# Kernel optimization log

Measured on AMD Instinct MI355X. Metric: run time of the kernel, lower is better.

## Reference

```python
import jax, jax.numpy as jnp
import numpy as np

RES = 512
RANK = 48
OUT = 32
N = 1_000_000
INIT = 0.1


def _contract_linf(xyz, aabb):
    # L-infinity cuboid contraction of unbounded coords into [-1,1]^3.
    center = (aabb[:3] + aabb[3:]) * 0.5
    half = jnp.maximum((aabb[3:] - aabb[:3]) * 0.5, 1e-6)
    x = (xyz - center) / half
    linf = jnp.max(jnp.abs(x), axis=-1, keepdims=True)
    safe = jnp.maximum(linf, 1.0)
    scale = jnp.where(linf > 1.0, (2.0 - 1.0 / safe) / safe, 1.0)
    return jnp.clip(x * scale, -1.0, 1.0)


def _sample_plane(plane, gx, gy):
    # plane: [R, Res, Res]; gx,gy in [-1,1] shape [N]; bilinear, align_corners=True.
    res = plane.shape[-1]
    fx = (gx + 1.0) * 0.5 * (res - 1)
    fy = (gy + 1.0) * 0.5 * (res - 1)
    x0 = jnp.clip(jnp.floor(fx), 0, res - 2).astype(jnp.int32)
    y0 = jnp.clip(jnp.floor(fy), 0, res - 2).astype(jnp.int32)
    wx = fx - x0
    wy = fy - y0
    x1 = x0 + 1
    y1 = y0 + 1
    # gathers -> [R, N]
    v = (plane[:, y0, x0] * ((1 - wy) * (1 - wx))
         + plane[:, y0, x1] * ((1 - wy) * wx)
         + plane[:, y1, x0] * (wy * (1 - wx))
         + plane[:, y1, x1] * (wy * wx))
    return v


def _sample_line(line, g):
    # line: [R, Res]; 1-D linear interp along the resolution axis (align_corners=True).
    res = line.shape[-1]
    f = (g + 1.0) * 0.5 * (res - 1)
    i0 = jnp.clip(jnp.floor(f), 0, res - 2).astype(jnp.int32)
    w = f - i0
    return line[:, i0] * (1 - w) + line[:, i0 + 1] * w  # [R, N]


def setup_inputs() -> dict:
    key = jax.random.key(0)
    ks = jax.random.split(key, 9)
    coordinates = jax.random.normal(ks[0], (N, 3), dtype=jnp.float32) * 1.5  # some points outside aabb
    aabb = jnp.array([-1.0, -1.0, -1.0, 1.0, 1.0, 1.0], dtype=jnp.float32)
    plane_xy = jax.random.normal(ks[1], (RANK, RES, RES), dtype=jnp.float32) * INIT
    plane_xz = jax.random.normal(ks[2], (RANK, RES, RES), dtype=jnp.float32) * INIT
    plane_yz = jax.random.normal(ks[3], (RANK, RES, RES), dtype=jnp.float32) * INIT
    line_z = jax.random.normal(ks[4], (RANK, RES), dtype=jnp.float32) * INIT
    line_y = jax.random.normal(ks[5], (RANK, RES), dtype=jnp.float32) * INIT
    line_x = jax.random.normal(ks[6], (RANK, RES), dtype=jnp.float32) * INIT
    W = jax.random.normal(ks[7], (OUT, RANK), dtype=jnp.float32) * INIT
    b = jnp.zeros((OUT,), dtype=jnp.float32)
    return {"coordinates": coordinates, "aabb": aabb,
            "plane_xy": plane_xy, "plane_xz": plane_xz, "plane_yz": plane_yz,
            "line_z": line_z, "line_y": line_y, "line_x": line_x,
            "W": W, "b": b}


def reference(coordinates, aabb, plane_xy, plane_xz, plane_yz, line_z, line_y, line_x, W, b):
    c = _contract_linf(coordinates, aabb)  # [N,3] in [-1,1]
    cx, cy, cz = c[:, 0], c[:, 1], c[:, 2]
    # VM decomposition: plane(a,b) * line(c), summed over the three permutations -> [R, N]
    vm = (_sample_plane(plane_xy, cx, cy) * _sample_line(line_z, cz)
          + _sample_plane(plane_xz, cx, cz) * _sample_line(line_y, cy)
          + _sample_plane(plane_yz, cy, cz) * _sample_line(line_x, cx))
    # projection rank -> out_channels: [N, OUT]
    return jnp.einsum('rn,or->no', vm, W) + b
```

## Files before the change

### kernel.cpp

```cpp
#include <hip/hip_runtime.h>
#include <stdint.h>

#define RES 512
#define RANK 48
#define OUT_CH 32
#define KBITS 5
#define NBKT (1 << (3 * KBITS))
#define STR 24

typedef unsigned int u32;
typedef unsigned short u16;
typedef u32 u32x4 __attribute__((ext_vector_type(4)));


static __device__ __forceinline__ u16 f2bf(float f){
  u32 u = __float_as_uint(f);
  u32 r = (u + 0x7fffu + ((u >> 16) & 1u)) >> 16;
  return (u16)r;
}

struct PS { int off; float w00, w01, w10, w11; };
static __device__ __forceinline__ PS plane_setup(float gx, float gy){
  float fx = (gx + 1.f) * 255.5f;
  float fy = (gy + 1.f) * 255.5f;
  float x0f = fminf(fmaxf(floorf(fx), 0.f), 510.f);
  float y0f = fminf(fmaxf(floorf(fy), 0.f), 510.f);
  float wx = fx - x0f, wy = fy - y0f;
  PS s;
  s.off = (int)y0f * RES + (int)x0f;
  float ux = 1.f - wx, uy = 1.f - wy;
  s.w00 = uy * ux; s.w01 = uy * wx; s.w10 = wy * ux; s.w11 = wy * wx;
  return s;
}

struct LS { int off; float w; };
static __device__ __forceinline__ LS line_setup(float g){
  float f = (g + 1.f) * 255.5f;
  float i0f = fminf(fmaxf(floorf(f), 0.f), 510.f);
  LS s; s.off = (int)i0f; s.w = f - i0f;
  return s;
}

static __device__ __forceinline__ void contract(const float* __restrict__ aabb,
                                                float px, float py, float pz,
                                                float& cx, float& cy, float& cz){
  float c0 = (aabb[0] + aabb[3]) * 0.5f;
  float c1 = (aabb[1] + aabb[4]) * 0.5f;
  float c2 = (aabb[2] + aabb[5]) * 0.5f;
  float h0 = fmaxf((aabb[3] - aabb[0]) * 0.5f, 1e-6f);
  float h1 = fmaxf((aabb[4] - aabb[1]) * 0.5f, 1e-6f);
  float h2 = fmaxf((aabb[5] - aabb[2]) * 0.5f, 1e-6f);
  float x0 = (px - c0) / h0;
  float x1 = (py - c1) / h1;
  float x2 = (pz - c2) / h2;
  float linf = fmaxf(fabsf(x0), fmaxf(fabsf(x1), fabsf(x2)));
  float scale = 1.f;
  if (linf > 1.f){ float inv = 1.f / linf; scale = (2.f - inv) * inv; }
  cx = fminf(fmaxf(x0 * scale, -1.f), 1.f);
  cy = fminf(fmaxf(x1 * scale, -1.f), 1.f);
  cz = fminf(fmaxf(x2 * scale, -1.f), 1.f);
}

static __device__ __forceinline__ u32 spread3(u32 x){
  x &= 0x3FF;
  x = (x | (x << 16)) & 0x030000FF;
  x = (x | (x <<  8)) & 0x0300F00F;
  x = (x | (x <<  4)) & 0x030C30C3;
  x = (x | (x <<  2)) & 0x09249249;
  return x;
}

static __device__ __forceinline__ u32 morton_key(float cx, float cy, float cz){
  u32 kx = (u32)fminf(fmaxf((cx + 1.f) * 16.f, 0.f), 31.f);
  u32 ky = (u32)fminf(fmaxf((cy + 1.f) * 16.f, 0.f), 31.f);
  u32 kz = (u32)fminf(fmaxf((cz + 1.f) * 16.f, 0.f), 31.f);
  return spread3(kx) | (spread3(ky) << 1) | (spread3(kz) << 2);
}


__global__ void zero_hist(u32* __restrict__ hist)
{
  hist[blockIdx.x * 1024 + threadIdx.x] = 0u;
}


#define TRANS_P 3072
#define TRANS_L 6

__global__ void prep_fused(const float* __restrict__ pxy, const float* __restrict__ pxz,
                           const float* __restrict__ pyz,
                           const float* __restrict__ lz, const float* __restrict__ ly,
                           const float* __restrict__ lx,
                           const float* __restrict__ coords, const float* __restrict__ aabb,
                           u32* __restrict__ dstP, u32* __restrict__ dstL,
                           u32* __restrict__ hist, u32* __restrict__ keyrank, int n)
{
  __shared__ u32 lds[256 * 25];
  int bid = blockIdx.x;
  int tid = threadIdx.x;
  if (bid < TRANS_P){
    int xh = bid & 1, y = (bid >> 1) & 511, p = bid >> 10;
    const float* src = (p == 0) ? pxy : (p == 1) ? pxz : pyz;
    int x = xh * 256 + tid;
    #pragma unroll
    for (int r2 = 0; r2 < 24; ++r2){
      float f0 = src[((size_t)(2 * r2) * RES + y) * RES + x];
      float f1 = src[((size_t)(2 * r2 + 1) * RES + y) * RES + x];
      lds[tid * 25 + r2] = (u32)f2bf(f0) | ((u32)f2bf(f1) << 16);
    }
    __syncthreads();
    u32* dplane = dstP + (size_t)p * (RES * RES * STR);
    size_t base = ((size_t)y * RES + xh * 256) * STR;
    for (int t = tid; t < 256 * STR; t += 256){
      dplane[base + t] = lds[t + t / 24];
    }
  } else if (bid < TRANS_P + TRANS_L){
    int g = (bid - TRANS_P) * 256 + tid;
    if (g < 3 * RES){
      int p = g >> 9, i = g & 511;
      const float* src = (p == 0) ? lz : (p == 1) ? ly : lx;
      u32* d = dstL + (size_t)g * STR;
      #pragma unroll
      for (int r2 = 0; r2 < 24; ++r2){
        float f0 = src[(2 * r2) * RES + i];
        float f1 = src[(2 * r2 + 1) * RES + i];
        d[r2] = (u32)f2bf(f0) | ((u32)f2bf(f1) << 16);
      }
    }
  } else {
    int i = (bid - TRANS_P - TRANS_L) * 256 + tid;
    if (i < n){
      float cx, cy, cz;
      contract(aabb, coords[3*i], coords[3*i+1], coords[3*i+2], cx, cy, cz);
      u32 key = morton_key(cx, cy, cz);
      u32 rank = atomicAdd(hist + key, 1u);
      keyrank[i] = (rank << 15) | key;
    }
  }
}


__global__ void scan_kernel(u32* __restrict__ hist)
{
  __shared__ u32 part[1024];
  int tid = threadIdx.x;
  int base = tid * 32;
  u32 loc[32];
  u32 s = 0;
  #pragma unroll
  for (int j = 0; j < 32; j++){ loc[j] = hist[base + j]; s += loc[j]; }
  part[tid] = s;
  __syncthreads();
  for (int off = 1; off < 1024; off <<= 1){
    u32 v = 0;
    if (tid >= off) v = part[tid - off];
    __syncthreads();
    part[tid] += v;
    __syncthreads();
  }
  u32 run = part[tid] - s;
  #pragma unroll
  for (int j = 0; j < 32; j++){ u32 t = loc[j]; hist[base + j] = run; run += t; }
}


__global__ void key_scatter(const float* __restrict__ coords, const float* __restrict__ aabb,
                            const u32* __restrict__ base, const u32* __restrict__ keyrank,
                            float4* __restrict__ sorted, int n)
{
  int i = blockIdx.x * 256 + threadIdx.x;
  if (i >= n) return;
  float cx, cy, cz;
  contract(aabb, coords[3*i], coords[3*i+1], coords[3*i+2], cx, cy, cz);
  u32 kr = keyrank[i];
  u32 pos = base[kr & 0x7FFFu] + (kr >> 15);
  sorted[pos] = make_float4(cx, cy, cz, __uint_as_float((u32)i));
}


#define EXLO(u) __uint_as_float((u) << 16)
#define EXHI(u) __uint_as_float((u) & 0xffff0000u)

#define DO_ELEM(EX, RIDX) do{ \
  float pa = fmaf(EX(a00[jj]), sa.w00, fmaf(EX(a01[jj]), sa.w01, fmaf(EX(a10[jj]), sa.w10, EX(a11[jj]) * sa.w11))); \
  float pb = fmaf(EX(b00[jj]), sb.w00, fmaf(EX(b01[jj]), sb.w01, fmaf(EX(b10[jj]), sb.w10, EX(b11[jj]) * sb.w11))); \
  float pc = fmaf(EX(c00[jj]), sc.w00, fmaf(EX(c01[jj]), sc.w01, fmaf(EX(c10[jj]), sc.w10, EX(c11[jj]) * sc.w11))); \
  float lzv = fmaf(tz.w, EX(vz1[jj]) - EX(vz0[jj]), EX(vz0[jj])); \
  float lyv = fmaf(ty.w, EX(vy1[jj]) - EX(vy0[jj]), EX(vy0[jj])); \
  float lxv = fmaf(tx.w, EX(vx1[jj]) - EX(vx0[jj]), EX(vx0[jj])); \
  float vm = fmaf(pa, lzv, fmaf(pb, lyv, pc * lxv)); \
  const float4* wrow = Wt4 + (RIDX) * 8; \
  _Pragma("unroll") for (int q = 0; q < 8; q++){ float4 w4 = wrow[q]; \
    acc[4*q+0] = fmaf(vm, w4.x, acc[4*q+0]); acc[4*q+1] = fmaf(vm, w4.y, acc[4*q+1]); \
    acc[4*q+2] = fmaf(vm, w4.z, acc[4*q+2]); acc[4*q+3] = fmaf(vm, w4.w, acc[4*q+3]); } \
}while(0)

static __device__ __forceinline__ void geo_compute(float cx, float cy, float cz,
    const u32* __restrict__ pl, const u32* __restrict__ ln,
    const float* __restrict__ Wt, const float* __restrict__ bias,
    float* __restrict__ acc)
{
  PS sa = plane_setup(cx, cy);
  PS sb = plane_setup(cx, cz);
  PS sc = plane_setup(cy, cz);
  LS tz = line_setup(cz);
  LS ty = line_setup(cy);
  LS tx = line_setup(cx);

  const u32* P0 = pl + (size_t)sa.off * STR;
  const u32* P1 = pl + (size_t)RES * RES * STR     + (size_t)sb.off * STR;
  const u32* P2 = pl + (size_t)2 * RES * RES * STR + (size_t)sc.off * STR;
  const u32* LZp = ln +                          (size_t)tz.off * STR;
  const u32* LYp = ln + (size_t)RES * STR     + (size_t)ty.off * STR;
  const u32* LXp = ln + (size_t)2 * RES * STR + (size_t)tx.off * STR;

  #pragma unroll
  for (int o = 0; o < 8; o++){
    float4 bv = *(const float4*)(bias + o * 4);
    acc[4*o+0] = bv.x; acc[4*o+1] = bv.y; acc[4*o+2] = bv.z; acc[4*o+3] = bv.w;
  }
  const float4* Wt4 = (const float4*)Wt;

  #pragma unroll 2
  for (int ch = 0; ch < 6; ++ch){
    const int bo = ch * 4;
    u32x4 a00 = *(const u32x4*)(P0 + bo);
    u32x4 a01 = *(const u32x4*)(P0 + STR + bo);
    u32x4 a10 = *(const u32x4*)(P0 + RES * STR + bo);
    u32x4 a11 = *(const u32x4*)(P0 + RES * STR + STR + bo);
    u32x4 b00 = *(const u32x4*)(P1 + bo);
    u32x4 b01 = *(const u32x4*)(P1 + STR + bo);
    u32x4 b10 = *(const u32x4*)(P1 + RES * STR + bo);
    u32x4 b11 = *(const u32x4*)(P1 + RES * STR + STR + bo);
    u32x4 c00 = *(const u32x4*)(P2 + bo);
    u32x4 c01 = *(const u32x4*)(P2 + STR + bo);
    u32x4 c10 = *(const u32x4*)(P2 + RES * STR + bo);
    u32x4 c11 = *(const u32x4*)(P2 + RES * STR + STR + bo);
    u32x4 vz0 = *(const u32x4*)(LZp + bo);
    u32x4 vz1 = *(const u32x4*)(LZp + STR + bo);
    u32x4 vy0 = *(const u32x4*)(LYp + bo);
    u32x4 vy1 = *(const u32x4*)(LYp + STR + bo);
    u32x4 vx0 = *(const u32x4*)(LXp + bo);
    u32x4 vx1 = *(const u32x4*)(LXp + STR + bo);

    #pragma unroll
    for (int jj = 0; jj < 4; jj++){
      DO_ELEM(EXLO, ch * 8 + jj * 2);
      DO_ELEM(EXHI, ch * 8 + jj * 2 + 1);
    }
  }
}


__global__ __launch_bounds__(256, 2)
void geo_sorted(const float4* __restrict__ sorted,
                const u32* __restrict__ pl, const u32* __restrict__ ln,
                const float* __restrict__ W, const float* __restrict__ bias,
                float* __restrict__ out, int n, int nwg)
{
  __shared__ __align__(16) float Wt[RANK * OUT_CH];
  for (int t = threadIdx.x; t < RANK * OUT_CH; t += 256){
    int r = t >> 5, o = t & 31;
    Wt[t] = W[o * RANK + r];
  }
  __syncthreads();

  int bid = blockIdx.x;
  int q = nwg >> 3, r8 = nwg & 7;
  int xcd = bid & 7, sub = bid >> 3;
  int swz = (xcd < r8 ? xcd * (q + 1) : r8 * (q + 1) + (xcd - r8) * q) + sub;

  int i = swz * 256 + threadIdx.x;
  if (i >= n) return;

  u32x4 pr = __builtin_nontemporal_load((const u32x4*)(sorted + i));
  float cx = __uint_as_float(pr[0]);
  float cy = __uint_as_float(pr[1]);
  float cz = __uint_as_float(pr[2]);
  u32 oidx = pr[3];

  float acc[OUT_CH];
  geo_compute(cx, cy, cz, pl, ln, Wt, bias, acc);

  float4* o4 = (float4*)(out + (size_t)oidx * 32);
  #pragma unroll
  for (int qq = 0; qq < 8; qq++)
    o4[qq] = make_float4(acc[4*qq+0], acc[4*qq+1], acc[4*qq+2], acc[4*qq+3]);
}


__global__ __launch_bounds__(256, 2)
void geo_unsorted(const float* __restrict__ coords, const float* __restrict__ aabb,
                  const u32* __restrict__ pl, const u32* __restrict__ ln,
                  const float* __restrict__ W, const float* __restrict__ bias,
                  float* __restrict__ out, int n)
{
  __shared__ __align__(16) float Wt[RANK * OUT_CH];
  for (int t = threadIdx.x; t < RANK * OUT_CH; t += 256){
    int r = t >> 5, o = t & 31;
    Wt[t] = W[o * RANK + r];
  }
  __syncthreads();

  int i = blockIdx.x * 256 + threadIdx.x;
  if (i >= n) return;

  float cx, cy, cz;
  contract(aabb, coords[3*i], coords[3*i+1], coords[3*i+2], cx, cy, cz);

  float acc[OUT_CH];
  geo_compute(cx, cy, cz, pl, ln, Wt, bias, acc);

  float4* o4 = (float4*)(out + (size_t)i * 32);
  #pragma unroll
  for (int qq = 0; qq < 8; qq++)
    o4[qq] = make_float4(acc[4*qq+0], acc[4*qq+1], acc[4*qq+2], acc[4*qq+3]);
}


__global__ __launch_bounds__(256, 2)
void geo_direct(const float* __restrict__ coords, const float* __restrict__ aabb,
                const float* __restrict__ PXY, const float* __restrict__ PXZ, const float* __restrict__ PYZ,
                const float* __restrict__ LZ, const float* __restrict__ LY, const float* __restrict__ LX,
                const float* __restrict__ W, const float* __restrict__ bias,
                float* __restrict__ out, int n)
{
  __shared__ __align__(16) float Wt[RANK * OUT_CH];
  for (int t = threadIdx.x; t < RANK * OUT_CH; t += 256){
    int r = t >> 5, o = t & 31;
    Wt[t] = W[o * RANK + r];
  }
  __syncthreads();

  int i = blockIdx.x * 256 + threadIdx.x;
  if (i >= n) return;

  float cx, cy, cz;
  contract(aabb, coords[3*i], coords[3*i+1], coords[3*i+2], cx, cy, cz);

  PS sa = plane_setup(cx, cy);
  PS sb = plane_setup(cx, cz);
  PS sc = plane_setup(cy, cz);
  LS tz = line_setup(cz);
  LS ty = line_setup(cy);
  LS tx = line_setup(cx);

  float acc[OUT_CH];
  #pragma unroll
  for (int o = 0; o < 8; o++){
    float4 bv = *(const float4*)(bias + o * 4);
    acc[4*o+0] = bv.x; acc[4*o+1] = bv.y; acc[4*o+2] = bv.z; acc[4*o+3] = bv.w;
  }
  const float4* Wt4 = (const float4*)Wt;

  for (int r = 0; r < RANK; r++){
    const float* pA = PXY + (size_t)r * RES * RES;
    const float* pB = PXZ + (size_t)r * RES * RES;
    const float* pC = PYZ + (size_t)r * RES * RES;
    float va = fmaf(pA[sa.off], sa.w00, fmaf(pA[sa.off+1], sa.w01, fmaf(pA[sa.off+RES], sa.w10, pA[sa.off+RES+1]*sa.w11)));
    float vb = fmaf(pB[sb.off], sb.w00, fmaf(pB[sb.off+1], sb.w01, fmaf(pB[sb.off+RES], sb.w10, pB[sb.off+RES+1]*sb.w11)));
    float vc = fmaf(pC[sc.off], sc.w00, fmaf(pC[sc.off+1], sc.w01, fmaf(pC[sc.off+RES], sc.w10, pC[sc.off+RES+1]*sc.w11)));
    float l0;
    l0 = LZ[r * RES + tz.off];
    float lzv = fmaf(tz.w, LZ[r * RES + tz.off + 1] - l0, l0);
    l0 = LY[r * RES + ty.off];
    float lyv = fmaf(ty.w, LY[r * RES + ty.off + 1] - l0, l0);
    l0 = LX[r * RES + tx.off];
    float lxv = fmaf(tx.w, LX[r * RES + tx.off + 1] - l0, l0);
    float vm = fmaf(va, lzv, fmaf(vb, lyv, vc * lxv));
    const float4* wrow = Wt4 + r * 8;
    #pragma unroll
    for (int q = 0; q < 8; q++){
      float4 w4 = wrow[q];
      acc[4*q+0] = fmaf(vm, w4.x, acc[4*q+0]); acc[4*q+1] = fmaf(vm, w4.y, acc[4*q+1]);
      acc[4*q+2] = fmaf(vm, w4.z, acc[4*q+2]); acc[4*q+3] = fmaf(vm, w4.w, acc[4*q+3]);
    }
  }

  float4* o4 = (float4*)(out + (size_t)i * 32);
  #pragma unroll
  for (int q = 0; q < 8; q++)
    o4[q] = make_float4(acc[4*q+0], acc[4*q+1], acc[4*q+2], acc[4*q+3]);
}


extern "C" void kernel_launch(void* const* d_in, const int* in_sizes, int n_in,
                              void* d_out, int out_size, void* d_ws, size_t ws_size,
                              hipStream_t stream)
{
  const float* coords = (const float*)d_in[0];
  const float* aabb   = (const float*)d_in[1];
  const float* pxy    = (const float*)d_in[2];
  const float* pxz    = (const float*)d_in[3];
  const float* pyz    = (const float*)d_in[4];
  const float* lz     = (const float*)d_in[5];
  const float* ly     = (const float*)d_in[6];
  const float* lx     = (const float*)d_in[7];
  const float* W      = (const float*)d_in[8];
  const float* bias   = (const float*)d_in[9];
  float* out = (float*)d_out;
  int n = in_sizes[0] / 3;
  int nwg = (n + 255) / 256;

  const size_t planesU = (size_t)3 * RES * RES * STR;
  const size_t linesU  = (size_t)3 * RES * STR;
  const size_t histU   = NBKT;
  const size_t keyrU   = (size_t)n;
  const size_t sortedU = (size_t)4 * n;
  const size_t needFull = (planesU + linesU + histU + keyrU + sortedU) * 4;

  if (ws_size >= needFull){
    u32* pl      = (u32*)d_ws;
    u32* ln      = pl + planesU;
    u32* hist    = ln + linesU;
    u32* keyrank = hist + histU;
    float4* sorted = (float4*)(keyrank + keyrU);
    zero_hist<<<NBKT / 1024, 1024, 0, stream>>>(hist);
    prep_fused<<<TRANS_P + TRANS_L + nwg, 256, 0, stream>>>(
        pxy, pxz, pyz, lz, ly, lx, coords, aabb, pl, ln, hist, keyrank, n);
    scan_kernel<<<1, 1024, 0, stream>>>(hist);
    key_scatter<<<nwg, 256, 0, stream>>>(coords, aabb, hist, keyrank, sorted, n);
    geo_sorted<<<nwg, 256, 0, stream>>>(sorted, pl, ln, W, bias, out, n, nwg);
  } else if (ws_size >= (planesU + linesU) * 4){
    u32* pl = (u32*)d_ws;
    u32* ln = pl + planesU;
    prep_fused<<<TRANS_P + TRANS_L, 256, 0, stream>>>(
        pxy, pxz, pyz, lz, ly, lx, coords, aabb, pl, ln, (u32*)pl, (u32*)pl, 0);
    geo_unsorted<<<nwg, 256, 0, stream>>>(coords, aabb, pl, ln, W, bias, out, n);
  } else {
    geo_direct<<<nwg, 256, 0, stream>>>(coords, aabb, pxy, pxz, pyz, lz, ly, lx, W, bias, out, n);
  }
}
```

Before: 413.8 us.

## Bucket points by clamped-axis class and skip zero-weight corner loads

Points are classified by whether a contracted coordinate sits exactly on a clamped boundary, where one bilinear or linear weight is exactly 0 or 1. That class goes into the sort key ahead of the Morton code, so wavefronts are grouped by class. The kernel then picks a templated specialization per wavefront that skips the gather loads for zero-weight plane corners and line endpoints. This cuts memory gathers for the many points outside the box, whose contraction lands on the boundary. In exchange the histogram is seven times larger, the scan is wider, and key and rank now go to separate arrays, all of which add prep traffic.

New measurement: 869.6 us. 110% more time.

```diff
diff --git a/kernel.cpp b/kernel.cpp
--- a/kernel.cpp
+++ b/kernel.cpp
@@ -5,7 +5,9 @@
 #define RANK 48
 #define OUT_CH 32
 #define KBITS 5
-#define NBKT (1 << (3 * KBITS))
+#define NMORT (1 << (3 * KBITS))
+#define NCLS 7
+#define NBKT2 (NCLS * NMORT)
 #define STR 24
 
 typedef unsigned int u32;
@@ -19,26 +21,10 @@
   return (u16)r;
 }
 
-struct PS { int off; float w00, w01, w10, w11; };
-static __device__ __forceinline__ PS plane_setup(float gx, float gy){
-  float fx = (gx + 1.f) * 255.5f;
-  float fy = (gy + 1.f) * 255.5f;
-  float x0f = fminf(fmaxf(floorf(fx), 0.f), 510.f);
-  float y0f = fminf(fmaxf(floorf(fy), 0.f), 510.f);
-  float wx = fx - x0f, wy = fy - y0f;
-  PS s;
-  s.off = (int)y0f * RES + (int)x0f;
-  float ux = 1.f - wx, uy = 1.f - wy;
-  s.w00 = uy * ux; s.w01 = uy * wx; s.w10 = wy * ux; s.w11 = wy * wx;
-  return s;
-}
-
-struct LS { int off; float w; };
-static __device__ __forceinline__ LS line_setup(float g){
-  float f = (g + 1.f) * 255.5f;
-  float i0f = fminf(fmaxf(floorf(f), 0.f), 510.f);
-  LS s; s.off = (int)i0f; s.w = f - i0f;
-  return s;
+static __device__ __forceinline__ void axis_setup(float c, int& o, float& w){
+  float f = (c + 1.f) * 255.5f;
+  float of = fminf(fmaxf(floorf(f), 0.f), 510.f);
+  o = (int)of; w = f - of;
 }
 
 static __device__ __forceinline__ void contract(const float* __restrict__ aabb,
@@ -77,6 +63,12 @@
   return spread3(kx) | (spread3(ky) << 1) | (spread3(kz) << 2);
 }
 
+static __device__ __forceinline__ u32 classify(float wx, float wy, float wz){
+  return (wx == 1.f) ? 0u : (wx == 0.f) ? 1u :
+         (wy == 1.f) ? 2u : (wy == 0.f) ? 3u :
+         (wz == 1.f) ? 4u : (wz == 0.f) ? 5u : 6u;
+}
+
 
 __global__ void zero_hist(u32* __restrict__ hist)
 {
@@ -93,7 +85,8 @@
                            const float* __restrict__ lx,
                            const float* __restrict__ coords, const float* __restrict__ aabb,
                            u32* __restrict__ dstP, u32* __restrict__ dstL,
-                           u32* __restrict__ hist, u32* __restrict__ keyrank, int n)
+                           u32* __restrict__ hist, u32* __restrict__ keyA,
+                           u32* __restrict__ rankA, int n)
 {
   __shared__ u32 lds[256 * 25];
   int bid = blockIdx.x;
@@ -132,9 +125,11 @@
     if (i < n){
       float cx, cy, cz;
       contract(aabb, coords[3*i], coords[3*i+1], coords[3*i+2], cx, cy, cz);
-      u32 key = morton_key(cx, cy, cz);
-      u32 rank = atomicAdd(hist + key, 1u);
-      keyrank[i] = (rank << 15) | key;
+      int ox, oy, oz; float wx, wy, wz;
+      axis_setup(cx, ox, wx); axis_setup(cy, oy, wy); axis_setup(cz, oz, wz);
+      u32 key = (classify(wx, wy, wz) << 15) | morton_key(cx, cy, cz);
+      keyA[i] = key;
+      rankA[i] = atomicAdd(hist + key, 1u);
     }
   }
 }
@@ -143,12 +138,11 @@
 __global__ void scan_kernel(u32* __restrict__ hist)
 {
   __shared__ u32 part[1024];
+  const int PER4 = NBKT2 / 1024 / 4;
   int tid = threadIdx.x;
-  int base = tid * 32;
-  u32 loc[32];
+  uint4* h4 = (uint4*)hist + (size_t)tid * PER4;
   u32 s = 0;
-  #pragma unroll
-  for (int j = 0; j < 32; j++){ loc[j] = hist[base + j]; s += loc[j]; }
+  for (int j = 0; j < PER4; ++j){ uint4 v = h4[j]; s += v.x + v.y + v.z + v.w; }
   part[tid] = s;
   __syncthreads();
   for (int off = 1; off < 1024; off <<= 1){
@@ -159,21 +153,26 @@
     __syncthreads();
   }
   u32 run = part[tid] - s;
-  #pragma unroll
-  for (int j = 0; j < 32; j++){ u32 t = loc[j]; hist[base + j] = run; run += t; }
+  for (int j = 0; j < PER4; ++j){
+    uint4 v = h4[j], o;
+    o.x = run; run += v.x;
+    o.y = run; run += v.y;
+    o.z = run; run += v.z;
+    o.w = run; run += v.w;
+    h4[j] = o;
+  }
 }
 
 
 __global__ void key_scatter(const float* __restrict__ coords, const float* __restrict__ aabb,
-                            const u32* __restrict__ base, const u32* __restrict__ keyrank,
-                            float4* __restrict__ sorted, int n)
+                            const u32* __restrict__ base, const u32* __restrict__ keyA,
+                            const u32* __restrict__ rankA, float4* __restrict__ sorted, int n)
 {
   int i = blockIdx.x * 256 + threadIdx.x;
   if (i >= n) return;
   float cx, cy, cz;
   contract(aabb, coords[3*i], coords[3*i+1], coords[3*i+2], cx, cy, cz);
-  u32 kr = keyrank[i];
-  u32 pos = base[kr & 0x7FFFu] + (kr >> 15);
+  u32 pos = base[keyA[i]] + rankA[i];
   sorted[pos] = make_float4(cx, cy, cz, __uint_as_float((u32)i));
 }
 
@@ -181,13 +180,16 @@
 #define EXLO(u) __uint_as_float((u) << 16)
 #define EXHI(u) __uint_as_float((u) & 0xffff0000u)
 
+#define LOADC(name, FLAG, addr) \
+  u32x4 name = {0,0,0,0}; if constexpr (FLAG){ name = *(const u32x4*)(addr); }
+
 #define DO_ELEM(EX, RIDX) do{ \
-  float pa = fmaf(EX(a00[jj]), sa.w00, fmaf(EX(a01[jj]), sa.w01, fmaf(EX(a10[jj]), sa.w10, EX(a11[jj]) * sa.w11))); \
-  float pb = fmaf(EX(b00[jj]), sb.w00, fmaf(EX(b01[jj]), sb.w01, fmaf(EX(b10[jj]), sb.w10, EX(b11[jj]) * sb.w11))); \
-  float pc = fmaf(EX(c00[jj]), sc.w00, fmaf(EX(c01[jj]), sc.w01, fmaf(EX(c10[jj]), sc.w10, EX(c11[jj]) * sc.w11))); \
-  float lzv = fmaf(tz.w, EX(vz1[jj]) - EX(vz0[jj]), EX(vz0[jj])); \
-  float lyv = fmaf(ty.w, EX(vy1[jj]) - EX(vy0[jj]), EX(vy0[jj])); \
-  float lxv = fmaf(tx.w, EX(vx1[jj]) - EX(vx0[jj]), EX(vx0[jj])); \
+  float pa = fmaf(EX(a00[jj]), aw00, fmaf(EX(a01[jj]), aw01, fmaf(EX(a10[jj]), aw10, EX(a11[jj]) * aw11))); \
+  float pb = fmaf(EX(b00[jj]), bw00, fmaf(EX(b01[jj]), bw01, fmaf(EX(b10[jj]), bw10, EX(b11[jj]) * bw11))); \
+  float pc = fmaf(EX(c00[jj]), cw00, fmaf(EX(c01[jj]), cw01, fmaf(EX(c10[jj]), cw10, EX(c11[jj]) * cw11))); \
+  float lzv = fmaf(wz, EX(vz1[jj]) - EX(vz0[jj]), EX(vz0[jj])); \
+  float lyv = fmaf(wy, EX(vy1[jj]) - EX(vy0[jj]), EX(vy0[jj])); \
+  float lxv = fmaf(wx, EX(vx1[jj]) - EX(vx0[jj]), EX(vx0[jj])); \
   float vm = fmaf(pa, lzv, fmaf(pb, lyv, pc * lxv)); \
   const float4* wrow = Wt4 + (RIDX) * 8; \
   _Pragma("unroll") for (int q = 0; q < 8; q++){ float4 w4 = wrow[q]; \
@@ -195,24 +197,37 @@
     acc[4*q+2] = fmaf(vm, w4.z, acc[4*q+2]); acc[4*q+3] = fmaf(vm, w4.w, acc[4*q+3]); } \
 }while(0)
 
-static __device__ __forceinline__ void geo_compute(float cx, float cy, float cz,
+template<int CLS>
+static __device__ __forceinline__ void geo_core(int ox, int oy, int oz,
+    float wx, float wy, float wz,
     const u32* __restrict__ pl, const u32* __restrict__ ln,
     const float* __restrict__ Wt, const float* __restrict__ bias,
     float* __restrict__ acc)
 {
-  PS sa = plane_setup(cx, cy);
-  PS sb = plane_setup(cx, cz);
-  PS sc = plane_setup(cy, cz);
-  LS tz = line_setup(cz);
-  LS ty = line_setup(cy);
-  LS tx = line_setup(cx);
-
-  const u32* P0 = pl + (size_t)sa.off * STR;
-  const u32* P1 = pl + (size_t)RES * RES * STR     + (size_t)sb.off * STR;
-  const u32* P2 = pl + (size_t)2 * RES * RES * STR + (size_t)sc.off * STR;
-  const u32* LZp = ln +                          (size_t)tz.off * STR;
-  const u32* LYp = ln + (size_t)RES * STR     + (size_t)ty.off * STR;
-  const u32* LXp = ln + (size_t)2 * RES * STR + (size_t)tx.off * STR;
+  constexpr bool SXP = (CLS == 0), SXM = (CLS == 1);
+  constexpr bool SYP = (CLS == 2), SYM = (CLS == 3);
+  constexpr bool SZP = (CLS == 4), SZM = (CLS == 5);
+  constexpr bool LA00 = !(SXP || SYP), LA01 = !(SXM || SYP);
+  constexpr bool LA10 = !(SXP || SYM), LA11 = !(SXM || SYM);
+  constexpr bool LB00 = !(SXP || SZP), LB01 = !(SXM || SZP);
+  constexpr bool LB10 = !(SXP || SZM), LB11 = !(SXM || SZM);
+  constexpr bool LC00 = !(SYP || SZP), LC01 = !(SYM || SZP);
+  constexpr bool LC10 = !(SYP || SZM), LC11 = !(SYM || SZM);
+  constexpr bool LZ0 = !SZP, LZ1 = !SZM;
+  constexpr bool LY0 = !SYP, LY1 = !SYM;
+  constexpr bool LX0 = !SXP, LX1 = !SXM;
+
+  float uxw = 1.f - wx, uyw = 1.f - wy, uzw = 1.f - wz;
+  float aw00 = uyw * uxw, aw01 = uyw * wx, aw10 = wy * uxw, aw11 = wy * wx;
+  float bw00 = uzw * uxw, bw01 = uzw * wx, bw10 = wz * uxw, bw11 = wz * wx;
+  float cw00 = uzw * uyw, cw01 = uzw * wy, cw10 = wz * uyw, cw11 = wz * wy;
+
+  const u32* P0 = pl + ((size_t)oy * RES + ox) * STR;
+  const u32* P1 = pl + (size_t)RES * RES * STR     + ((size_t)oz * RES + ox) * STR;
+  const u32* P2 = pl + (size_t)2 * RES * RES * STR + ((size_t)oz * RES + oy) * STR;
+  const u32* LZp = ln +                          (size_t)oz * STR;
+  const u32* LYp = ln + (size_t)RES * STR     + (size_t)oy * STR;
+  const u32* LXp = ln + (size_t)2 * RES * STR + (size_t)ox * STR;
 
   #pragma unroll
   for (int o = 0; o < 8; o++){
@@ -224,24 +239,24 @@
   #pragma unroll 2
   for (int ch = 0; ch < 6; ++ch){
     const int bo = ch * 4;
-    u32x4 a00 = *(const u32x4*)(P0 + bo);
-    u32x4 a01 = *(const u32x4*)(P0 + STR + bo);
-    u32x4 a10 = *(const u32x4*)(P0 + RES * STR + bo);
-    u32x4 a11 = *(const u32x4*)(P0 + RES * STR + STR + bo);
-    u32x4 b00 = *(const u32x4*)(P1 + bo);
-    u32x4 b01 = *(const u32x4*)(P1 + STR + bo);
-    u32x4 b10 = *(const u32x4*)(P1 + RES * STR + bo);
-    u32x4 b11 = *(const u32x4*)(P1 + RES * STR + STR + bo);
-    u32x4 c00 = *(const u32x4*)(P2 + bo);
-    u32x4 c01 = *(const u32x4*)(P2 + STR + bo);
-    u32x4 c10 = *(const u32x4*)(P2 + RES * STR + bo);
-    u32x4 c11 = *(const u32x4*)(P2 + RES * STR + STR + bo);
-    u32x4 vz0 = *(const u32x4*)(LZp + bo);
-    u32x4 vz1 = *(const u32x4*)(LZp + STR + bo);
-    u32x4 vy0 = *(const u32x4*)(LYp + bo);
-    u32x4 vy1 = *(const u32x4*)(LYp + STR + bo);
-    u32x4 vx0 = *(const u32x4*)(LXp + bo);
-    u32x4 vx1 = *(const u32x4*)(LXp + STR + bo);
+    LOADC(a00, LA00, P0 + bo);
+    LOADC(a01, LA01, P0 + STR + bo);
+    LOADC(a10, LA10, P0 + RES * STR + bo);
+    LOADC(a11, LA11, P0 + RES * STR + STR + bo);
+    LOADC(b00, LB00, P1 + bo);
+    LOADC(b01, LB01, P1 + STR + bo);
+    LOADC(b10, LB10, P1 + RES * STR + bo);
+    LOADC(b11, LB11, P1 + RES * STR + STR + bo);
+    LOADC(c00, LC00, P2 + bo);
+    LOADC(c01, LC01, P2 + STR + bo);
+    LOADC(c10, LC10, P2 + RES * STR + bo);
+    LOADC(c11, LC11, P2 + RES * STR + STR + bo);
+    LOADC(vz0, LZ0, LZp + bo);
+    LOADC(vz1, LZ1, LZp + STR + bo);
+    LOADC(vy0, LY0, LYp + bo);
+    LOADC(vy1, LY1, LYp + STR + bo);
+    LOADC(vx0, LX0, LXp + bo);
+    LOADC(vx1, LX1, LXp + STR + bo);
 
     #pragma unroll
     for (int jj = 0; jj < 4; jj++){
@@ -279,8 +294,17 @@
   float cz = __uint_as_float(pr[2]);
   u32 oidx = pr[3];
 
+  int ox, oy, oz; float wx, wy, wz;
+  axis_setup(cx, ox, wx); axis_setup(cy, oy, wy); axis_setup(cz, oz, wz);
+
   float acc[OUT_CH];
-  geo_compute(cx, cy, cz, pl, ln, Wt, bias, acc);
+  if      (__all(wx == 1.f)) geo_core<0>(ox, oy, oz, wx, wy, wz, pl, ln, Wt, bias, acc);
+  else if (__all(wx == 0.f)) geo_core<1>(ox, oy, oz, wx, wy, wz, pl, ln, Wt, bias, acc);
+  else if (__all(wy == 1.f)) geo_core<2>(ox, oy, oz, wx, wy, wz, pl, ln, Wt, bias, acc);
+  else if (__all(wy == 0.f)) geo_core<3>(ox, oy, oz, wx, wy, wz, pl, ln, Wt, bias, acc);
+  else if (__all(wz == 1.f)) geo_core<4>(ox, oy, oz, wx, wy, wz, pl, ln, Wt, bias, acc);
+  else if (__all(wz == 0.f)) geo_core<5>(ox, oy, oz, wx, wy, wz, pl, ln, Wt, bias, acc);
+  else                       geo_core<6>(ox, oy, oz, wx, wy, wz, pl, ln, Wt, bias, acc);
 
   float4* o4 = (float4*)(out + (size_t)oidx * 32);
   #pragma unroll
@@ -307,9 +331,11 @@
 
   float cx, cy, cz;
   contract(aabb, coords[3*i], coords[3*i+1], coords[3*i+2], cx, cy, cz);
+  int ox, oy, oz; float wx, wy, wz;
+  axis_setup(cx, ox, wx); axis_setup(cy, oy, wy); axis_setup(cz, oz, wz);
 
   float acc[OUT_CH];
-  geo_compute(cx, cy, cz, pl, ln, Wt, bias, acc);
+  geo_core<6>(ox, oy, oz, wx, wy, wz, pl, ln, Wt, bias, acc);
 
   float4* o4 = (float4*)(out + (size_t)i * 32);
   #pragma unroll
@@ -337,13 +363,14 @@
 
   float cx, cy, cz;
   contract(aabb, coords[3*i], coords[3*i+1], coords[3*i+2], cx, cy, cz);
-
-  PS sa = plane_setup(cx, cy);
-  PS sb = plane_setup(cx, cz);
-  PS sc = plane_setup(cy, cz);
-  LS tz = line_setup(cz);
-  LS ty = line_setup(cy);
-  LS tx = line_setup(cx);
+  int ox, oy, oz; float wx, wy, wz;
+  axis_setup(cx, ox, wx); axis_setup(cy, oy, wy); axis_setup(cz, oz, wz);
+
+  int offA = oy * RES + ox, offB = oz * RES + ox, offC = oz * RES + oy;
+  float uxw = 1.f - wx, uyw = 1.f - wy, uzw = 1.f - wz;
+  float aw00 = uyw*uxw, aw01 = uyw*wx, aw10 = wy*uxw, aw11 = wy*wx;
+  float bw00 = uzw*uxw, bw01 = uzw*wx, bw10 = wz*uxw, bw11 = wz*wx;
+  float cw00 = uzw*uyw, cw01 = uzw*wy, cw10 = wz*uyw, cw11 = wz*wy;
 
   float acc[OUT_CH];
   #pragma unroll
@@ -357,16 +384,16 @@
     const float* pA = PXY + (size_t)r * RES * RES;
     const float* pB = PXZ + (size_t)r * RES * RES;
     const float* pC = PYZ + (size_t)r * RES * RES;
-    float va = fmaf(pA[sa.off], sa.w00, fmaf(pA[sa.off+1], sa.w01, fmaf(pA[sa.off+RES], sa.w10, pA[sa.off+RES+1]*sa.w11)));
-    float vb = fmaf(pB[sb.off], sb.w00, fmaf(pB[sb.off+1], sb.w01, fmaf(pB[sb.off+RES], sb.w10, pB[sb.off+RES+1]*sb.w11)));
-    float vc = fmaf(pC[sc.off], sc.w00, fmaf(pC[sc.off+1], sc.w01, fmaf(pC[sc.off+RES], sc.w10, pC[sc.off+RES+1]*sc.w11)));
+    float va = fmaf(pA[offA], aw00, fmaf(pA[offA+1], aw01, fmaf(pA[offA+RES], aw10, pA[offA+RES+1]*aw11)));
+    float vb = fmaf(pB[offB], bw00, fmaf(pB[offB+1], bw01, fmaf(pB[offB+RES], bw10, pB[offB+RES+1]*bw11)));
+    float vc = fmaf(pC[offC], cw00, fmaf(pC[offC+1], cw01, fmaf(pC[offC+RES], cw10, pC[offC+RES+1]*cw11)));
     float l0;
-    l0 = LZ[r * RES + tz.off];
-    float lzv = fmaf(tz.w, LZ[r * RES + tz.off + 1] - l0, l0);
-    l0 = LY[r * RES + ty.off];
-    float lyv = fmaf(ty.w, LY[r * RES + ty.off + 1] - l0, l0);
-    l0 = LX[r * RES + tx.off];
-    float lxv = fmaf(tx.w, LX[r * RES + tx.off + 1] - l0, l0);
+    l0 = LZ[r * RES + oz];
+    float lzv = fmaf(wz, LZ[r * RES + oz + 1] - l0, l0);
+    l0 = LY[r * RES + oy];
+    float lyv = fmaf(wy, LY[r * RES + oy + 1] - l0, l0);
+    l0 = LX[r * RES + ox];
+    float lxv = fmaf(wx, LX[r * RES + ox + 1] - l0, l0);
     float vm = fmaf(va, lzv, fmaf(vb, lyv, vc * lxv));
     const float4* wrow = Wt4 + r * 8;
     #pragma unroll
@@ -404,28 +431,30 @@
 
   const size_t planesU = (size_t)3 * RES * RES * STR;
   const size_t linesU  = (size_t)3 * RES * STR;
-  const size_t histU   = NBKT;
-  const size_t keyrU   = (size_t)n;
+  const size_t histU   = NBKT2;
+  const size_t keyU    = (size_t)n;
+  const size_t rankU   = (size_t)n;
   const size_t sortedU = (size_t)4 * n;
-  const size_t needFull = (planesU + linesU + histU + keyrU + sortedU) * 4;
+  const size_t needFull = (planesU + linesU + histU + keyU + rankU + sortedU) * 4;
 
   if (ws_size >= needFull){
-    u32* pl      = (u32*)d_ws;
-    u32* ln      = pl + planesU;
-    u32* hist    = ln + linesU;
-    u32* keyrank = hist + histU;
-    float4* sorted = (float4*)(keyrank + keyrU);
-    zero_hist<<<NBKT / 1024, 1024, 0, stream>>>(hist);
+    u32* pl    = (u32*)d_ws;
+    u32* ln    = pl + planesU;
+    u32* hist  = ln + linesU;
+    u32* keyA  = hist + histU;
+    u32* rankA = keyA + keyU;
+    float4* sorted = (float4*)(rankA + rankU);
+    zero_hist<<<NBKT2 / 1024, 1024, 0, stream>>>(hist);
     prep_fused<<<TRANS_P + TRANS_L + nwg, 256, 0, stream>>>(
-        pxy, pxz, pyz, lz, ly, lx, coords, aabb, pl, ln, hist, keyrank, n);
+        pxy, pxz, pyz, lz, ly, lx, coords, aabb, pl, ln, hist, keyA, rankA, n);
     scan_kernel<<<1, 1024, 0, stream>>>(hist);
-    key_scatter<<<nwg, 256, 0, stream>>>(coords, aabb, hist, keyrank, sorted, n);
+    key_scatter<<<nwg, 256, 0, stream>>>(coords, aabb, hist, keyA, rankA, sorted, n);
     geo_sorted<<<nwg, 256, 0, stream>>>(sorted, pl, ln, W, bias, out, n, nwg);
   } else if (ws_size >= (planesU + linesU) * 4){
     u32* pl = (u32*)d_ws;
     u32* ln = pl + planesU;
     prep_fused<<<TRANS_P + TRANS_L, 256, 0, stream>>>(
-        pxy, pxz, pyz, lz, ly, lx, coords, aabb, pl, ln, (u32*)pl, (u32*)pl, 0);
+        pxy, pxz, pyz, lz, ly, lx, coords, aabb, pl, ln, (u32*)pl, (u32*)pl, (u32*)pl, 0);
     geo_unsorted<<<nwg, 256, 0, stream>>>(coords, aabb, pl, ln, W, bias, out, n);
   } else {
     geo_direct<<<nwg, 256, 0, stream>>>(coords, aabb, pxy, pxz, pyz, lz, ly, lx, W, bias, out, n);
```

## Restructure sampling loop corner-by-corner with rank-wide accumulators and shared axis setup

Applied to the files above, without the earlier changes.

Axis floor and weight setup is now computed once per axis instead of once per plane/line pairing. The fused per-chunk gather-and-project loop is replaced by a corner-major pass: per-point arrays of 48 line values and 48 accumulators are built, each plane corner is folded in, and the 48-to-32 projection runs at the end. This lowers the number of loads in flight at once and reorganises the arithmetic. In exchange it holds about 96 extra floats live, which raises register pressure and may cut occupancy or cause spills.

New measurement: 365.4 us. -11.7%, faster.

```diff
diff --git a/kernel.cpp b/kernel.cpp
--- a/kernel.cpp
+++ b/kernel.cpp
@@ -19,26 +19,10 @@
   return (u16)r;
 }
 
-struct PS { int off; float w00, w01, w10, w11; };
-static __device__ __forceinline__ PS plane_setup(float gx, float gy){
-  float fx = (gx + 1.f) * 255.5f;
-  float fy = (gy + 1.f) * 255.5f;
-  float x0f = fminf(fmaxf(floorf(fx), 0.f), 510.f);
-  float y0f = fminf(fmaxf(floorf(fy), 0.f), 510.f);
-  float wx = fx - x0f, wy = fy - y0f;
-  PS s;
-  s.off = (int)y0f * RES + (int)x0f;
-  float ux = 1.f - wx, uy = 1.f - wy;
-  s.w00 = uy * ux; s.w01 = uy * wx; s.w10 = wy * ux; s.w11 = wy * wx;
-  return s;
-}
-
-struct LS { int off; float w; };
-static __device__ __forceinline__ LS line_setup(float g){
-  float f = (g + 1.f) * 255.5f;
-  float i0f = fminf(fmaxf(floorf(f), 0.f), 510.f);
-  LS s; s.off = (int)i0f; s.w = f - i0f;
-  return s;
+static __device__ __forceinline__ void axis_setup(float c, int& o, float& w){
+  float f = (c + 1.f) * 255.5f;
+  float of = fminf(fmaxf(floorf(f), 0.f), 510.f);
+  o = (int)of; w = f - of;
 }
 
 static __device__ __forceinline__ void contract(const float* __restrict__ aabb,
@@ -181,38 +165,74 @@
 #define EXLO(u) __uint_as_float((u) << 16)
 #define EXHI(u) __uint_as_float((u) & 0xffff0000u)
 
-#define DO_ELEM(EX, RIDX) do{ \
-  float pa = fmaf(EX(a00[jj]), sa.w00, fmaf(EX(a01[jj]), sa.w01, fmaf(EX(a10[jj]), sa.w10, EX(a11[jj]) * sa.w11))); \
-  float pb = fmaf(EX(b00[jj]), sb.w00, fmaf(EX(b01[jj]), sb.w01, fmaf(EX(b10[jj]), sb.w10, EX(b11[jj]) * sb.w11))); \
-  float pc = fmaf(EX(c00[jj]), sc.w00, fmaf(EX(c01[jj]), sc.w01, fmaf(EX(c10[jj]), sc.w10, EX(c11[jj]) * sc.w11))); \
-  float lzv = fmaf(tz.w, EX(vz1[jj]) - EX(vz0[jj]), EX(vz0[jj])); \
-  float lyv = fmaf(ty.w, EX(vy1[jj]) - EX(vy0[jj]), EX(vy0[jj])); \
-  float lxv = fmaf(tx.w, EX(vx1[jj]) - EX(vx0[jj]), EX(vx0[jj])); \
-  float vm = fmaf(pa, lzv, fmaf(pb, lyv, pc * lxv)); \
-  const float4* wrow = Wt4 + (RIDX) * 8; \
-  _Pragma("unroll") for (int q = 0; q < 8; q++){ float4 w4 = wrow[q]; \
-    acc[4*q+0] = fmaf(vm, w4.x, acc[4*q+0]); acc[4*q+1] = fmaf(vm, w4.y, acc[4*q+1]); \
-    acc[4*q+2] = fmaf(vm, w4.z, acc[4*q+2]); acc[4*q+3] = fmaf(vm, w4.w, acc[4*q+3]); } \
-}while(0)
-
-static __device__ __forceinline__ void geo_compute(float cx, float cy, float cz,
+static __device__ __forceinline__ void build_lv(float lv[RANK], const u32* __restrict__ p, float w){
+  #pragma unroll
+  for (int j = 0; j < 6; j++){
+    u32x4 a = *(const u32x4*)(p + 4 * j);
+    u32x4 b = *(const u32x4*)(p + STR + 4 * j);
+    #pragma unroll
+    for (int k = 0; k < 4; k++){
+      int r = (j * 4 + k) * 2;
+      float lo0 = EXLO(a[k]), hi0 = EXHI(a[k]);
+      float lo1 = EXLO(b[k]), hi1 = EXHI(b[k]);
+      lv[r]     = fmaf(w, lo1 - lo0, lo0);
+      lv[r + 1] = fmaf(w, hi1 - hi0, hi0);
+    }
+  }
+}
+
+static __device__ __forceinline__ void acc_corner(float vm[RANK], const float lv[RANK],
+                                                  const u32* __restrict__ p, float wc){
+  #pragma unroll
+  for (int j = 0; j < 6; j++){
+    u32x4 t = *(const u32x4*)(p + 4 * j);
+    #pragma unroll
+    for (int k = 0; k < 4; k++){
+      int r = (j * 4 + k) * 2;
+      vm[r]     = fmaf(EXLO(t[k]) * lv[r],     wc, vm[r]);
+      vm[r + 1] = fmaf(EXHI(t[k]) * lv[r + 1], wc, vm[r + 1]);
+    }
+  }
+}
+
+static __device__ __forceinline__ void geo_core(int ox, int oy, int oz,
+    float wx, float wy, float wz,
     const u32* __restrict__ pl, const u32* __restrict__ ln,
     const float* __restrict__ Wt, const float* __restrict__ bias,
     float* __restrict__ acc)
 {
-  PS sa = plane_setup(cx, cy);
-  PS sb = plane_setup(cx, cz);
-  PS sc = plane_setup(cy, cz);
-  LS tz = line_setup(cz);
-  LS ty = line_setup(cy);
-  LS tx = line_setup(cx);
-
-  const u32* P0 = pl + (size_t)sa.off * STR;
-  const u32* P1 = pl + (size_t)RES * RES * STR     + (size_t)sb.off * STR;
-  const u32* P2 = pl + (size_t)2 * RES * RES * STR + (size_t)sc.off * STR;
-  const u32* LZp = ln +                          (size_t)tz.off * STR;
-  const u32* LYp = ln + (size_t)RES * STR     + (size_t)ty.off * STR;
-  const u32* LXp = ln + (size_t)2 * RES * STR + (size_t)tx.off * STR;
+  float uxw = 1.f - wx, uyw = 1.f - wy, uzw = 1.f - wz;
+
+  const u32* A  = pl + ((size_t)oy * RES + ox) * STR;
+  const u32* B  = pl + (size_t)RES * RES * STR     + ((size_t)oz * RES + ox) * STR;
+  const u32* C  = pl + (size_t)2 * RES * RES * STR + ((size_t)oz * RES + oy) * STR;
+  const u32* LZp = ln +                          (size_t)oz * STR;
+  const u32* LYp = ln + (size_t)RES * STR     + (size_t)oy * STR;
+  const u32* LXp = ln + (size_t)2 * RES * STR + (size_t)ox * STR;
+
+  float vm[RANK];
+  #pragma unroll
+  for (int r = 0; r < RANK; r++) vm[r] = 0.f;
+
+  float lv[RANK];
+
+  build_lv(lv, LZp, wz);
+  acc_corner(vm, lv, A,                  uyw * uxw);
+  acc_corner(vm, lv, A + STR,            uyw * wx);
+  acc_corner(vm, lv, A + RES * STR,      wy * uxw);
+  acc_corner(vm, lv, A + RES * STR + STR, wy * wx);
+
+  build_lv(lv, LYp, wy);
+  acc_corner(vm, lv, B,                  uzw * uxw);
+  acc_corner(vm, lv, B + STR,            uzw * wx);
+  acc_corner(vm, lv, B + RES * STR,      wz * uxw);
+  acc_corner(vm, lv, B + RES * STR + STR, wz * wx);
+
+  build_lv(lv, LXp, wx);
+  acc_corner(vm, lv, C,                  uzw * uyw);
+  acc_corner(vm, lv, C + STR,            uzw * wy);
+  acc_corner(vm, lv, C + RES * STR,      wz * uyw);
+  acc_corner(vm, lv, C + RES * STR + STR, wz * wy);
 
   #pragma unroll
   for (int o = 0; o < 8; o++){
@@ -220,33 +240,15 @@
     acc[4*o+0] = bv.x; acc[4*o+1] = bv.y; acc[4*o+2] = bv.z; acc[4*o+3] = bv.w;
   }
   const float4* Wt4 = (const float4*)Wt;
-
-  #pragma unroll 2
-  for (int ch = 0; ch < 6; ++ch){
-    const int bo = ch * 4;
-    u32x4 a00 = *(const u32x4*)(P0 + bo);
-    u32x4 a01 = *(const u32x4*)(P0 + STR + bo);
-    u32x4 a10 = *(const u32x4*)(P0 + RES * STR + bo);
-    u32x4 a11 = *(const u32x4*)(P0 + RES * STR + STR + bo);
-    u32x4 b00 = *(const u32x4*)(P1 + bo);
-    u32x4 b01 = *(const u32x4*)(P1 + STR + bo);
-    u32x4 b10 = *(const u32x4*)(P1 + RES * STR + bo);
-    u32x4 b11 = *(const u32x4*)(P1 + RES * STR + STR + bo);
-    u32x4 c00 = *(const u32x4*)(P2 + bo);
-    u32x4 c01 = *(const u32x4*)(P2 + STR + bo);
-    u32x4 c10 = *(const u32x4*)(P2 + RES * STR + bo);
-    u32x4 c11 = *(const u32x4*)(P2 + RES * STR + STR + bo);
-    u32x4 vz0 = *(const u32x4*)(LZp + bo);
-    u32x4 vz1 = *(const u32x4*)(LZp + STR + bo);
-    u32x4 vy0 = *(const u32x4*)(LYp + bo);
-    u32x4 vy1 = *(const u32x4*)(LYp + STR + bo);
-    u32x4 vx0 = *(const u32x4*)(LXp + bo);
-    u32x4 vx1 = *(const u32x4*)(LXp + STR + bo);
-
+  #pragma unroll
+  for (int r = 0; r < RANK; r++){
+    float v = vm[r];
+    const float4* wrow = Wt4 + r * 8;
     #pragma unroll
-    for (int jj = 0; jj < 4; jj++){
-      DO_ELEM(EXLO, ch * 8 + jj * 2);
-      DO_ELEM(EXHI, ch * 8 + jj * 2 + 1);
+    for (int q = 0; q < 8; q++){
+      float4 w4 = wrow[q];
+      acc[4*q+0] = fmaf(v, w4.x, acc[4*q+0]); acc[4*q+1] = fmaf(v, w4.y, acc[4*q+1]);
+      acc[4*q+2] = fmaf(v, w4.z, acc[4*q+2]); acc[4*q+3] = fmaf(v, w4.w, acc[4*q+3]);
     }
   }
 }
@@ -279,8 +281,11 @@
   float cz = __uint_as_float(pr[2]);
   u32 oidx = pr[3];
 
+  int ox, oy, oz; float wx, wy, wz;
+  axis_setup(cx, ox, wx); axis_setup(cy, oy, wy); axis_setup(cz, oz, wz);
+
   float acc[OUT_CH];
-  geo_compute(cx, cy, cz, pl, ln, Wt, bias, acc);
+  geo_core(ox, oy, oz, wx, wy, wz, pl, ln, Wt, bias, acc);
 
   float4* o4 = (float4*)(out + (size_t)oidx * 32);
   #pragma unroll
@@ -307,9 +312,11 @@
 
   float cx, cy, cz;
   contract(aabb, coords[3*i], coords[3*i+1], coords[3*i+2], cx, cy, cz);
+  int ox, oy, oz; float wx, wy, wz;
+  axis_setup(cx, ox, wx); axis_setup(cy, oy, wy); axis_setup(cz, oz, wz);
 
   float acc[OUT_CH];
-  geo_compute(cx, cy, cz, pl, ln, Wt, bias, acc);
+  geo_core(ox, oy, oz, wx, wy, wz, pl, ln, Wt, bias, acc);
 
   float4* o4 = (float4*)(out + (size_t)i * 32);
   #pragma unroll
@@ -337,13 +344,14 @@
 
   float cx, cy, cz;
   contract(aabb, coords[3*i], coords[3*i+1], coords[3*i+2], cx, cy, cz);
-
-  PS sa = plane_setup(cx, cy);
-  PS sb = plane_setup(cx, cz);
-  PS sc = plane_setup(cy, cz);
-  LS tz = line_setup(cz);
-  LS ty = line_setup(cy);
-  LS tx = line_setup(cx);
+  int ox, oy, oz; float wx, wy, wz;
+  axis_setup(cx, ox, wx); axis_setup(cy, oy, wy); axis_setup(cz, oz, wz);
+
+  int offA = oy * RES + ox, offB = oz * RES + ox, offC = oz * RES + oy;
+  float uxw = 1.f - wx, uyw = 1.f - wy, uzw = 1.f - wz;
+  float aw00 = uyw*uxw, aw01 = uyw*wx, aw10 = wy*uxw, aw11 = wy*wx;
+  float bw00 = uzw*uxw, bw01 = uzw*wx, bw10 = wz*uxw, bw11 = wz*wx;
+  float cw00 = uzw*uyw, cw01 = uzw*wy, cw10 = wz*uyw, cw11 = wz*wy;
 
   float acc[OUT_CH];
   #pragma unroll
@@ -357,16 +365,16 @@
     const float* pA = PXY + (size_t)r * RES * RES;
     const float* pB = PXZ + (size_t)r * RES * RES;
     const float* pC = PYZ + (size_t)r * RES * RES;
-    float va = fmaf(pA[sa.off], sa.w00, fmaf(pA[sa.off+1], sa.w01, fmaf(pA[sa.off+RES], sa.w10, pA[sa.off+RES+1]*sa.w11)));
-    float vb = fmaf(pB[sb.off], sb.w00, fmaf(pB[sb.off+1], sb.w01, fmaf(pB[sb.off+RES], sb.w10, pB[sb.off+RES+1]*sb.w11)));
-    float vc = fmaf(pC[sc.off], sc.w00, fmaf(pC[sc.off+1], sc.w01, fmaf(pC[sc.off+RES], sc.w10, pC[sc.off+RES+1]*sc.w11)));
+    float va = fmaf(pA[offA], aw00, fmaf(pA[offA+1], aw01, fmaf(pA[offA+RES], aw10, pA[offA+RES+1]*aw11)));
+    float vb = fmaf(pB[offB], bw00, fmaf(pB[offB+1], bw01, fmaf(pB[offB+RES], bw10, pB[offB+RES+1]*bw11)));
+    float vc = fmaf(pC[offC], cw00, fmaf(pC[offC+1], cw01, fmaf(pC[offC+RES], cw10, pC[offC+RES+1]*cw11)));
     float l0;
-    l0 = LZ[r * RES + tz.off];
-    float lzv = fmaf(tz.w, LZ[r * RES + tz.off + 1] - l0, l0);
-    l0 = LY[r * RES + ty.off];
-    float lyv = fmaf(ty.w, LY[r * RES + ty.off + 1] - l0, l0);
-    l0 = LX[r * RES + tx.off];
-    float lxv = fmaf(tx.w, LX[r * RES + tx.off + 1] - l0, l0);
+    l0 = LZ[r * RES + oz];
+    float lzv = fmaf(wz, LZ[r * RES + oz + 1] - l0, l0);
+    l0 = LY[r * RES + oy];
+    float lyv = fmaf(wy, LY[r * RES + oy + 1] - l0, l0);
+    l0 = LX[r * RES + ox];
+    float lxv = fmaf(wx, LX[r * RES + ox + 1] - l0, l0);
     float vm = fmaf(va, lzv, fmaf(vb, lyv, vc * lxv));
     const float4* wrow = Wt4 + r * 8;
     #pragma unroll
```
